# Kernel tuning notes

Hardware: AMD Instinct MI355X
Metric: run time of the kernel (lower is better)

The kernel has to match this reference:

```python
import jax, jax.numpy as jnp
import numpy as np

# dims: batch, nodes, d_node, d_edge, d_attn_hid, heads, d_node_hid, d_edge_hid, layers
B, N, DN, DE, DH, H, DNH, DEH, L = 2, 256, 128, 64, 128, 8, 512, 256, 2
DHH = DH // H  # per-head dim
SCALE = 1.0 / (DH ** 0.5)  # source scales by full d_hid, not per-head dim


def _ln(x, g, b):
    m = jnp.mean(x, -1, keepdims=True)
    v = jnp.mean((x - m) ** 2, -1, keepdims=True)
    return (x - m) * jax.lax.rsqrt(v + 1e-5) * g + b


def _gelu(x):
    return jax.nn.gelu(x, approximate=False)  # torch nn.GELU default = exact erf


def setup_inputs() -> dict:
    key = jax.random.key(0)
    ks = iter(jax.random.split(key, 40))
    def w(shape, scale=0.02):
        return jax.random.normal(next(ks), shape, jnp.float32) * scale
    return {
        "node_features": jax.random.normal(next(ks), (B, N, DN), jnp.float32),
        "edge_features": jax.random.normal(next(ks), (B, N, N, DE), jnp.float32),
        "Wqkv_n": w((L, DN, 3 * DH)),
        "Wqkv_e": w((L, DE, 4 * DH)),
        "Wo": w((L, DH, DN)), "bo": jnp.zeros((L, DN), jnp.float32),
        "Wl0": w((L, DN, DN)), "bl0": jnp.zeros((L, DN), jnp.float32),
        "ln0_g": jnp.ones((L, DN), jnp.float32), "ln0_b": jnp.zeros((L, DN), jnp.float32),
        "Wm1": w((L, DN, DNH)), "Wm2": w((L, DNH, DN)), "bm2": jnp.zeros((L, DN), jnp.float32),
        "ln1_g": jnp.ones((L, DN), jnp.float32), "ln1_b": jnp.zeros((L, DN), jnp.float32),
        "We0": w((L, 2 * DE, DEH)), "be0": jnp.zeros((L, DEH), jnp.float32),
        "Ws": w((L, DN, DEH)), "bs": jnp.zeros((L, DEH), jnp.float32),
        "Wt": w((L, DN, DEH)), "bt": jnp.zeros((L, DEH), jnp.float32),
        "We1": w((L, DEH, DE)), "be1": jnp.zeros((L, DE), jnp.float32),
        "eln0_g": jnp.ones((L, DE), jnp.float32), "eln0_b": jnp.zeros((L, DE), jnp.float32),
        "Wem1": w((L, DE, DEH)), "Wem2": w((L, DEH, DE)), "bem2": jnp.zeros((L, DE), jnp.float32),
        "eln1_g": jnp.ones((L, DE), jnp.float32), "eln1_b": jnp.zeros((L, DE), jnp.float32),
    }


def _forward(node_features, edge_features, Wqkv_n, Wqkv_e, Wo, bo, Wl0, bl0,
             ln0_g, ln0_b, Wm1, Wm2, bm2, ln1_g, ln1_b, We0, be0, Ws, bs, Wt, bt,
             We1, be1, eln0_g, eln0_b, Wem1, Wem2, bem2, eln1_g, eln1_b):
    x, e = node_features, edge_features
    for l in range(L):
        # --- RTAttention (modulate_v=True, eval mode) ---
        qkv_n = (x @ Wqkv_n[l]).reshape(B, N, H, 3 * DHH).transpose(0, 2, 1, 3)  # b h n 3d
        qn, kn, vn = jnp.split(qkv_n, 3, axis=-1)
        qkv_e = (e @ Wqkv_e[l]).reshape(B, N, N, H, 4 * DHH).transpose(0, 3, 1, 2, 4)  # b h i j 4d
        eq, ek, ev, em = jnp.split(qkv_e, 4, axis=-1)
        q = qn[:, :, :, None, :] + eq            # b h i j d
        k = kn[:, :, None, :, :] + ek            # b h i j d
        v = vn[:, :, None, :, :] * em + ev       # modulated values
        dots = SCALE * jnp.einsum('bhijd,bhijd->bhij', q, k)
        attn = jax.nn.softmax(dots, axis=-1)
        out = jnp.einsum('bhij,bhijd->bhid', attn, v)
        out = out.transpose(0, 2, 1, 3).reshape(B, N, DH)
        attn_out = out @ Wo[l] + bo[l]
        # --- node updates: ln(x + lin0(attn)); ln(x + mlp(x)) ---
        x = _ln(x + (attn_out @ Wl0[l] + bl0[l]), ln0_g[l], ln0_b[l])
        x = _ln(x + (_gelu(x @ Wm1[l]) @ Wm2[l] + bm2[l]), ln1_g[l], ln1_b[l])
        # --- edge updates (EdgeLayer) ---
        src = (x @ Ws[l] + bs[l])[:, :, None, :]   # broadcast over target j
        tgt = (x @ Wt[l] + bt[l])[:, None, :, :]   # broadcast over source i
        ecat = jnp.concatenate([e, e.transpose(0, 2, 1, 3)], axis=-1)  # [e_ij, e_ji]
        h = _gelu(ecat @ We0[l] + be0[l] + src + tgt)
        e = _ln(e + (h @ We1[l] + be1[l]), eln0_g[l], eln0_b[l])
        e = _ln(e + (_gelu(e @ Wem1[l]) @ Wem2[l] + bem2[l]), eln1_g[l], eln1_b[l])
    return x, e


def reference(node_features, edge_features, Wqkv_n, Wqkv_e, Wo, bo, Wl0, bl0,
              ln0_g, ln0_b, Wm1, Wm2, bm2, ln1_g, ln1_b, We0, be0, Ws, bs, Wt, bt,
              We1, be1, eln0_g, eln0_b, Wem1, Wem2, bem2, eln1_g, eln1_b):
    return _forward(node_features, edge_features, Wqkv_n, Wqkv_e, Wo, bo, Wl0, bl0,
                    ln0_g, ln0_b, Wm1, Wm2, bm2, ln1_g, ln1_b, We0, be0, Ws, bs, Wt, bt,
                    We1, be1, eln0_g, eln0_b, Wem1, Wem2, bem2, eln1_g, eln1_b)
```

## Files before the change

kernel.cpp:

```cpp
#include <hip/hip_runtime.h>
#include <hip/hip_bf16.h>
#include <stdint.h>

#define BB 2
#define NN 256
#define DN 128
#define DE 64
#define DH 128
#define NH 8
#define DHH 16
#define DNH 512
#define DEH 256
#define NL 2
#define SCALE_ATT 0.08838834764831845f

typedef __hip_bfloat16 bf16;
typedef __attribute__((ext_vector_type(8))) short short8;
typedef __attribute__((ext_vector_type(4))) float f32x4;

__device__ __forceinline__ float gelu_f(float x) {
  return 0.5f * x * (1.0f + erff(x * 0.70710678118654752f));
}
__device__ __forceinline__ float gelu_t(float x) {
  float m2u = x * fmaf(x * x, -0.07135481627f, -1.59576912161f);
  float e = __expf(m2u);
  return x * __builtin_amdgcn_rcpf(1.f + e);
}

__device__ __forceinline__ float wave_sum(float v) {
#pragma unroll
  for (int o = 32; o > 0; o >>= 1) v += __shfl_xor(v, o, 64);
  return v;
}

__device__ __forceinline__ short f2bf(float f) {
  union { float f; uint32_t u; } v{f};
  uint32_t r = (v.u + 0x7FFFu + ((v.u >> 16) & 1u)) >> 16;
  return (short)r;
}
__device__ __forceinline__ float bf2f(short s) {
  union { uint32_t u; float f; } v;
  v.u = ((uint32_t)(uint16_t)s) << 16;
  return v.f;
}

__device__ __forceinline__ int hswz(int m, int n) {
  return m * 256 + (n ^ ((m & 7) << 3));
}

__global__ void k_detect(const uint32_t* g8, const uint32_t* g13, int* flag) {
  if (threadIdx.x == 0 && blockIdx.x == 0) {
    uint32_t a = g8[0], b = g13[0];
    *flag = (a == 0x3F803F80u || b == 0x3F803F80u) ? 1 : 0;
  }
}

struct CastArgs {
  const void* src[30];
  float* dst[30];
  int n[30];
  const int* flag;
};

__global__ __launch_bounds__(256) void k_cast_all(CastArgs a) {
  int ti = blockIdx.y;
  float* d = a.dst[ti];
  int n = a.n[ti];
  int stride = gridDim.x * blockDim.x;
  if (*a.flag) {
    const bf16* s = (const bf16*)a.src[ti];
    for (int i = blockIdx.x * blockDim.x + threadIdx.x; i < n; i += stride)
      d[i] = __bfloat162float(s[i]);
  } else {
    const float* s = (const float*)a.src[ti];
    for (int i = blockIdx.x * blockDim.x + threadIdx.x; i < n; i += stride)
      d[i] = s[i];
  }
}

__global__ __launch_bounds__(256) void k_cast_e(const void* __restrict__ src,
                                                short* __restrict__ dst,
                                                const int* __restrict__ flag) {
  const int n8 = BB * NN * NN * DE / 8;
  int stride = gridDim.x * blockDim.x;
  if (*flag) {
    const uint4* s = (const uint4*)src;
    uint4* d = (uint4*)dst;
    for (int i = blockIdx.x * blockDim.x + threadIdx.x; i < n8; i += stride) d[i] = s[i];
  } else {
    const float4* s = (const float4*)src;
    for (int i = blockIdx.x * blockDim.x + threadIdx.x; i < n8; i += stride) {
      float4 a = s[2 * i], b = s[2 * i + 1];
      short* o = dst + 8 * i;
      o[0] = f2bf(a.x); o[1] = f2bf(a.y); o[2] = f2bf(a.z); o[3] = f2bf(a.w);
      o[4] = f2bf(b.x); o[5] = f2bf(b.y); o[6] = f2bf(b.z); o[7] = f2bf(b.w);
    }
  }
}

__global__ __launch_bounds__(256) void k_cast_out(const float* __restrict__ x,
                                                  const short* __restrict__ e,
                                                  void* __restrict__ out_v,
                                                  const int* __restrict__ flag) {
  const int nx = BB * NN * DN;
  const int total = nx + BB * NN * NN * DE;
  int stride = gridDim.x * blockDim.x;
  if (*flag) {
    short* out = (short*)out_v;
    for (int i = blockIdx.x * blockDim.x + threadIdx.x; i < total; i += stride)
      out[i] = (i < nx) ? f2bf(x[i]) : e[i - nx];
  } else {
    float* out = (float*)out_v;
    for (int i = blockIdx.x * blockDim.x + threadIdx.x; i < total; i += stride)
      out[i] = (i < nx) ? x[i] : bf2f(e[i - nx]);
  }
}

struct WtJob { const float* src; short* dst; int K; int N; };
struct WtArgs { WtJob job[10]; };
__global__ __launch_bounds__(256) void k_wtrans_all(WtArgs a) {
  WtJob j = a.job[blockIdx.y];
  int total = j.K * j.N;
  int stride = gridDim.x * 256;
  for (int idx = blockIdx.x * 256 + threadIdx.x; idx < total; idx += stride) {
    int k = idx / j.N, n = idx - k * j.N;
    j.dst[n * j.K + k] = f2bf(j.src[idx]);
  }
}

__global__ __launch_bounds__(128) void k_node_qkv(const float* __restrict__ x,
                                                  const float* __restrict__ W,
                                                  float* __restrict__ qkv) {
  int row = blockIdx.x;
  __shared__ float xs[DN];
  int t = threadIdx.x;
  xs[t] = x[row * DN + t];
  __syncthreads();
#pragma unroll
  for (int c0 = 0; c0 < 384; c0 += 128) {
    int c = c0 + t;
    float a = 0.f;
    for (int k = 0; k < DN; ++k) a = fmaf(xs[k], W[k * 384 + c], a);
    qkv[row * 384 + c] = a;
  }
}

__global__ __launch_bounds__(256) void k_attn_fused(
    const short* __restrict__ e, const short* __restrict__ WqeT,
    const float* __restrict__ qkv, float* __restrict__ o_buf) {
  int i = blockIdx.x, hs = blockIdx.y, b = blockIdx.z;
  __shared__ float sp[4 * NN];
  int t = threadIdx.x;
  int wv = t >> 6, lane = t & 63, g8 = lane >> 4, lo = lane & 15;
  int h = hs * 4 + wv;
  const short* erow = e + (size_t)(b * NN + i) * NN * DE;
  size_t qbase = (size_t)(b * NN) * 384;

  float qv = qkv[(size_t)(b * NN + i) * 384 + h * 48 + lo];

  {
    short8 bq[2][2];
#pragma unroll
    for (int p = 0; p < 2; ++p)
#pragma unroll
      for (int ks = 0; ks < 2; ++ks)
        bq[p][ks] = *(const short8*)(
            WqeT + (size_t)((h * 4 + p) * 16 + lo) * 64 + ks * 32 + g8 * 8);
#pragma unroll 2
    for (int mt = 0; mt < 16; ++mt) {
      const short* ea = erow + (mt * 16 + lo) * DE;
      short8 a0 = *(const short8*)(ea + g8 * 8);
      short8 a1 = *(const short8*)(ea + 32 + g8 * 8);
      float kn4[4];
#pragma unroll
      for (int r = 0; r < 4; ++r)
        kn4[r] = qkv[qbase + (size_t)(mt * 16 + g8 * 4 + r) * 384 + h * 48 + 16 + lo];
      f32x4 cq = {0.f, 0.f, 0.f, 0.f}, ck = {0.f, 0.f, 0.f, 0.f};
      cq = __builtin_amdgcn_mfma_f32_16x16x32_bf16(a0, bq[0][0], cq, 0, 0, 0);
      cq = __builtin_amdgcn_mfma_f32_16x16x32_bf16(a1, bq[0][1], cq, 0, 0, 0);
      ck = __builtin_amdgcn_mfma_f32_16x16x32_bf16(a0, bq[1][0], ck, 0, 0, 0);
      ck = __builtin_amdgcn_mfma_f32_16x16x32_bf16(a1, bq[1][1], ck, 0, 0, 0);
#pragma unroll
      for (int r = 0; r < 4; ++r) {
        int j = mt * 16 + g8 * 4 + r;
        float s = (qv + cq[r]) * (kn4[r] + ck[r]);
#pragma unroll
        for (int off = 1; off < 16; off <<= 1) s += __shfl_xor(s, off, 64);
        if (lo == 0) sp[wv * NN + j] = s * SCALE_ATT;
      }
    }
  }

  {
    float v[4];
#pragma unroll
    for (int q = 0; q < 4; ++q) v[q] = sp[wv * NN + lane + 64 * q];
    float m = fmaxf(fmaxf(v[0], v[1]), fmaxf(v[2], v[3]));
#pragma unroll
    for (int o = 32; o > 0; o >>= 1) m = fmaxf(m, __shfl_xor(m, o, 64));
    float l = 0.f;
#pragma unroll
    for (int q = 0; q < 4; ++q) { v[q] = __expf(v[q] - m); l += v[q]; }
    l = wave_sum(l);
    float inv = 1.f / l;
#pragma unroll
    for (int q = 0; q < 4; ++q) sp[wv * NN + lane + 64 * q] = v[q] * inv;
  }

  {
    short8 bv[2][2];
#pragma unroll
    for (int p = 0; p < 2; ++p)
#pragma unroll
      for (int ks = 0; ks < 2; ++ks)
        bv[p][ks] = *(const short8*)(
            WqeT + (size_t)((h * 4 + 2 + p) * 16 + lo) * 64 + ks * 32 + g8 * 8);
    float oacc = 0.f;
#pragma unroll 2
    for (int mt = 0; mt < 16; ++mt) {
      const short* ea = erow + (mt * 16 + lo) * DE;
      short8 a0 = *(const short8*)(ea + g8 * 8);
      short8 a1 = *(const short8*)(ea + 32 + g8 * 8);
      float vn4[4];
#pragma unroll
      for (int r = 0; r < 4; ++r)
        vn4[r] = qkv[qbase + (size_t)(mt * 16 + g8 * 4 + r) * 384 + h * 48 + 32 + lo];
      f32x4 cv = {0.f, 0.f, 0.f, 0.f}, cm = {0.f, 0.f, 0.f, 0.f};
      cv = __builtin_amdgcn_mfma_f32_16x16x32_bf16(a0, bv[0][0], cv, 0, 0, 0);
      cv = __builtin_amdgcn_mfma_f32_16x16x32_bf16(a1, bv[0][1], cv, 0, 0, 0);
      cm = __builtin_amdgcn_mfma_f32_16x16x32_bf16(a0, bv[1][0], cm, 0, 0, 0);
      cm = __builtin_amdgcn_mfma_f32_16x16x32_bf16(a1, bv[1][1], cm, 0, 0, 0);
#pragma unroll
      for (int r = 0; r < 4; ++r) {
        int j = mt * 16 + g8 * 4 + r;
        float vv = fmaf(vn4[r], cm[r], cv[r]);
        oacc = fmaf(sp[wv * NN + j], vv, oacc);
      }
    }
    oacc += __shfl_xor(oacc, 16, 64);
    oacc += __shfl_xor(oacc, 32, 64);
    if (g8 == 0) o_buf[(size_t)(b * NN + i) * DH + h * 16 + lo] = oacc;
  }
}

__global__ __launch_bounds__(128) void k_node_fused(
    const float* __restrict__ o_buf,
    const float* __restrict__ Wo, const float* __restrict__ bo,
    const float* __restrict__ Wl0, const float* __restrict__ bl0,
    const float* __restrict__ g0, const float* __restrict__ b0n,
    const float* __restrict__ Wm1, const float* __restrict__ Wm2,
    const float* __restrict__ bm2, const float* __restrict__ g1,
    const float* __restrict__ b1n, const float* __restrict__ Ws,
    const float* __restrict__ bs, const float* __restrict__ Wt,
    const float* __restrict__ bt, const float* __restrict__ WqnN,
    float* __restrict__ qkv, float* __restrict__ srcb,
    float* __restrict__ tgtb, float* __restrict__ x) {
  int i = blockIdx.x, b = blockIdx.y;
  int row = b * NN + i;
  __shared__ float orow[DH];
  __shared__ float t1[DH];
  __shared__ float xs[DN];
  __shared__ float hs[DNH];
  __shared__ float red[4];
  int t = threadIdx.x;
  orow[t] = o_buf[(size_t)row * DH + t];
  __syncthreads();
  {
    float a = bo[t];
    for (int k = 0; k < DH; ++k) a = fmaf(orow[k], Wo[k * DN + t], a);
    t1[t] = a;
  }
  __syncthreads();
  {
    float y = bl0[t] + x[row * DN + t];
    for (int k = 0; k < DN; ++k) y = fmaf(t1[k], Wl0[k * DN + t], y);
    float s1 = wave_sum(y), s2 = wave_sum(y * y);
    if ((t & 63) == 0) { red[t >> 6] = s1; red[2 + (t >> 6)] = s2; }
    __syncthreads();
    float mean = (red[0] + red[1]) * (1.f / 128.f);
    float var = (red[2] + red[3]) * (1.f / 128.f) - mean * mean;
    float rr = rsqrtf(var + 1e-5f);
    xs[t] = (y - mean) * rr * g0[t] + b0n[t];
  }
  __syncthreads();
#pragma unroll
  for (int p = 0; p < 4; ++p) {
    int c = t + 128 * p;
    float a = 0.f;
    for (int k = 0; k < DN; ++k) a = fmaf(xs[k], Wm1[k * DNH + c], a);
    hs[c] = gelu_f(a);
  }
  __syncthreads();
  {
    float y = bm2[t] + xs[t];
    for (int k = 0; k < DNH; ++k) y = fmaf(hs[k], Wm2[k * DN + t], y);
    float s1 = wave_sum(y), s2 = wave_sum(y * y);
    if ((t & 63) == 0) { red[t >> 6] = s1; red[2 + (t >> 6)] = s2; }
    __syncthreads();
    float mean = (red[0] + red[1]) * (1.f / 128.f);
    float var = (red[2] + red[3]) * (1.f / 128.f) - mean * mean;
    float rr = rsqrtf(var + 1e-5f);
    float x2 = (y - mean) * rr * g1[t] + b1n[t];
    x[row * DN + t] = x2;
    xs[t] = x2;
  }
  __syncthreads();
#pragma unroll
  for (int half = 0; half < 2; ++half) {
    int c = t + 128 * half;
    float a = bs[c], cc = bt[c];
    for (int k = 0; k < DN; ++k) {
      float xv = xs[k];
      a = fmaf(xv, Ws[k * DEH + c], a);
      cc = fmaf(xv, Wt[k * DEH + c], cc);
    }
    srcb[(size_t)row * DEH + c] = a;
    tgtb[(size_t)row * DEH + c] = cc;
  }
  if (WqnN) {
#pragma unroll
    for (int p = 0; p < 3; ++p) {
      int c = t + 128 * p;
      float a = 0.f;
      for (int k = 0; k < DN; ++k) a = fmaf(xs[k], WqnN[k * 384 + c], a);
      qkv[(size_t)row * 384 + c] = a;
    }
  }
}

__global__ __launch_bounds__(256) void k_edge_fused(
    const short* __restrict__ e_in, const short* __restrict__ W0T,
    const float* __restrict__ b0, const short* __restrict__ W1T,
    const float* __restrict__ b1, const float* __restrict__ srcb,
    const float* __restrict__ tgtb, const float* __restrict__ g,
    const float* __restrict__ bb, const short* __restrict__ Wm1T,
    const short* __restrict__ Wm2T, const float* __restrict__ bm2,
    const float* __restrict__ gm, const float* __restrict__ bbm,
    short* __restrict__ e_out) {
  int jt = blockIdx.x, i = blockIdx.y, b = blockIdx.z;
  int j0 = jt * 64;
  __shared__ short hidT[64 * 256];
  int t = threadIdx.x;
  int wv = t >> 6, lane = t & 63, g8 = lane >> 4, lo = lane & 15;
  int nq = wv * 64;
  int m0 = wv * 16;

  {
    float bias_n[4];
#pragma unroll
    for (int nt = 0; nt < 4; ++nt)
      bias_n[nt] = b0[nq + nt * 16 + lo] + srcb[(size_t)(b * NN + i) * DEH + nq + nt * 16 + lo];
    short8 bfr1[4][4];
#pragma unroll
    for (int nt = 0; nt < 4; ++nt)
#pragma unroll
      for (int ks = 0; ks < 4; ++ks)
        bfr1[nt][ks] =
            *(const short8*)(W0T + (size_t)(nq + nt * 16 + lo) * 128 + ks * 32 + g8 * 8);
#pragma unroll
    for (int mt = 0; mt < 4; ++mt) {
      int mrow = mt * 16 + lo;
      float tg[4][4];
#pragma unroll
      for (int nt = 0; nt < 4; ++nt)
#pragma unroll
        for (int r = 0; r < 4; ++r)
          tg[nt][r] = tgtb[((size_t)(b * NN) + j0 + mt * 16 + g8 * 4 + r) * DEH +
                           nq + nt * 16 + lo];
      short8 a[4];
      const short* eA = e_in + ((size_t)(b * NN + i) * NN + j0 + mrow) * DE;
#pragma unroll
      for (int ks = 0; ks < 2; ++ks) a[ks] = *(const short8*)(eA + ks * 32 + g8 * 8);
      const short* eT = e_in + ((size_t)(b * NN + j0 + mrow) * NN + i) * DE;
#pragma unroll
      for (int ks = 0; ks < 2; ++ks) a[2 + ks] = *(const short8*)(eT + ks * 32 + g8 * 8);
      f32x4 acc[4];
#pragma unroll
      for (int nt = 0; nt < 4; ++nt) {
        f32x4 c = {0.f, 0.f, 0.f, 0.f};
#pragma unroll
        for (int ks = 0; ks < 4; ++ks)
          c = __builtin_amdgcn_mfma_f32_16x16x32_bf16(a[ks], bfr1[nt][ks], c, 0, 0, 0);
        acc[nt] = c;
      }
#pragma unroll
      for (int nt = 0; nt < 4; ++nt) {
        int n = nq + nt * 16 + lo;
#pragma unroll
        for (int r = 0; r < 4; ++r) {
          int m = mt * 16 + g8 * 4 + r;
          hidT[hswz(m, n)] = f2bf(gelu_t(acc[nt][r] + bias_n[nt] + tg[nt][r]));
        }
      }
    }
  }
  __syncthreads();

  float emid[4][4];
  {
    float resv[4][4];
#pragma unroll
    for (int nt = 0; nt < 4; ++nt)
#pragma unroll
      for (int r = 0; r < 4; ++r)
        resv[nt][r] = bf2f(e_in[((size_t)(b * NN + i) * NN + j0 + m0 + g8 * 4 + r) * DE +
                                nt * 16 + lo]);
    short8 a2[8];
#pragma unroll
    for (int ks = 0; ks < 8; ++ks)
      a2[ks] = *(const short8*)(hidT + hswz(m0 + lo, ks * 32 + g8 * 8));
    f32x4 acc2[4];
#pragma unroll
    for (int nt = 0; nt < 4; ++nt) {
      f32x4 c = {0.f, 0.f, 0.f, 0.f};
      const short* bp = W1T + (size_t)(nt * 16 + lo) * 256;
#pragma unroll
      for (int ks = 0; ks < 8; ++ks)
        c = __builtin_amdgcn_mfma_f32_16x16x32_bf16(
            a2[ks], *(const short8*)(bp + ks * 32 + g8 * 8), c, 0, 0, 0);
      acc2[nt] = c;
    }
#pragma unroll
    for (int nt = 0; nt < 4; ++nt) {
      int n = nt * 16 + lo;
      float bb1 = b1[n];
#pragma unroll
      for (int r = 0; r < 4; ++r) emid[nt][r] = acc2[nt][r] + bb1 + resv[nt][r];
    }
#pragma unroll
    for (int r = 0; r < 4; ++r) {
      float s = emid[0][r] + emid[1][r] + emid[2][r] + emid[3][r];
      float q = emid[0][r] * emid[0][r] + emid[1][r] * emid[1][r] +
                emid[2][r] * emid[2][r] + emid[3][r] * emid[3][r];
#pragma unroll
      for (int off = 1; off < 16; off <<= 1) {
        s += __shfl_xor(s, off, 64);
        q += __shfl_xor(q, off, 64);
      }
      float mean = s * (1.f / 64.f);
      float var = q * (1.f / 64.f) - mean * mean;
      float rr = rsqrtf(var + 1e-5f);
      int m = m0 + g8 * 4 + r;
#pragma unroll
      for (int nt = 0; nt < 4; ++nt) {
        int n = nt * 16 + lo;
        float v = (emid[nt][r] - mean) * rr * g[n] + bb[n];
        emid[nt][r] = v;
        hidT[hswz(m, n)] = f2bf(v);
      }
    }
  }

  {
    short8 a3[2];
#pragma unroll
    for (int ks = 0; ks < 2; ++ks)
      a3[ks] = *(const short8*)(hidT + hswz(m0 + lo, ks * 32 + g8 * 8));
#pragma unroll 4
    for (int nt = 0; nt < 16; ++nt) {
      f32x4 c = {0.f, 0.f, 0.f, 0.f};
      const short* bp = Wm1T + (size_t)(nt * 16 + lo) * 64;
#pragma unroll
      for (int ks = 0; ks < 2; ++ks)
        c = __builtin_amdgcn_mfma_f32_16x16x32_bf16(
            a3[ks], *(const short8*)(bp + ks * 32 + g8 * 8), c, 0, 0, 0);
      int n = nt * 16 + lo;
#pragma unroll
      for (int r = 0; r < 4; ++r)
        hidT[hswz(m0 + g8 * 4 + r, n)] = f2bf(gelu_t(c[r]));
    }
  }

  {
    short8 a4[8];
#pragma unroll
    for (int ks = 0; ks < 8; ++ks)
      a4[ks] = *(const short8*)(hidT + hswz(m0 + lo, ks * 32 + g8 * 8));
    f32x4 acc4[4];
#pragma unroll
    for (int nt = 0; nt < 4; ++nt) {
      f32x4 c = {0.f, 0.f, 0.f, 0.f};
      const short* bp = Wm2T + (size_t)(nt * 16 + lo) * 256;
#pragma unroll
      for (int ks = 0; ks < 8; ++ks)
        c = __builtin_amdgcn_mfma_f32_16x16x32_bf16(
            a4[ks], *(const short8*)(bp + ks * 32 + g8 * 8), c, 0, 0, 0);
      acc4[nt] = c;
    }
    float vals[4][4];
#pragma unroll
    for (int nt = 0; nt < 4; ++nt) {
      int n = nt * 16 + lo;
      float bv = bm2[n];
#pragma unroll
      for (int r = 0; r < 4; ++r) vals[nt][r] = acc4[nt][r] + bv + emid[nt][r];
    }
#pragma unroll
    for (int r = 0; r < 4; ++r) {
      float s = vals[0][r] + vals[1][r] + vals[2][r] + vals[3][r];
      float q = vals[0][r] * vals[0][r] + vals[1][r] * vals[1][r] +
                vals[2][r] * vals[2][r] + vals[3][r] * vals[3][r];
#pragma unroll
      for (int off = 1; off < 16; off <<= 1) {
        s += __shfl_xor(s, off, 64);
        q += __shfl_xor(q, off, 64);
      }
      float mean = s * (1.f / 64.f);
      float var = q * (1.f / 64.f) - mean * mean;
      float rr = rsqrtf(var + 1e-5f);
      int m = m0 + g8 * 4 + r;
#pragma unroll
      for (int nt = 0; nt < 4; ++nt) {
        int n = nt * 16 + lo;
        e_out[((size_t)(b * NN + i) * NN + j0 + m) * DE + n] =
            f2bf((vals[nt][r] - mean) * rr * gm[n] + bbm[n]);
      }
    }
  }
}

extern "C" void kernel_launch(void* const* d_in, const int* in_sizes, int n_in,
                              void* d_out, int out_size, void* d_ws, size_t ws_size,
                              hipStream_t stream) {
  float* ws = (float*)d_ws;
  int* flag = (int*)ws;
  size_t off = 64;
  auto alloc = [&](size_t n) {
    float* p = ws + off;
    off += (n + 63) & ~(size_t)63;
    return p;
  };
  float* x_f = alloc((size_t)BB * NN * DN);
  short* e_a = (short*)alloc((size_t)BB * NN * NN * DE / 2);
  short* e_b = (short*)alloc((size_t)BB * NN * NN * DE / 2);
  float* qkv = alloc((size_t)BB * NN * 384);
  float* o_buf = alloc((size_t)BB * NN * DH);
  float* srcb = alloc((size_t)BB * NN * DEH);
  float* tgtb = alloc((size_t)BB * NN * DEH);
  short* WqeT = (short*)alloc(NL * 512 * 64 / 2);
  short* We0T = (short*)alloc(NL * 256 * 128 / 2);
  short* We1T = (short*)alloc(NL * 64 * 256 / 2);
  short* Wem1T = (short*)alloc(NL * 256 * 64 / 2);
  short* Wem2T = (short*)alloc(NL * 64 * 256 / 2);

  float* wf[30];
  wf[0] = x_f;
  wf[1] = x_f;
  CastArgs ca;
  int ntens = n_in < 30 ? n_in : 30;
  for (int idx = 0; idx < ntens; ++idx) {
    if (idx >= 2) wf[idx] = alloc((size_t)in_sizes[idx]);
    ca.src[idx] = d_in[idx];
    ca.dst[idx] = wf[idx];
    ca.n[idx] = (idx == 1) ? 0 : in_sizes[idx];
  }
  ca.flag = flag;

  k_detect<<<1, 64, 0, stream>>>((const uint32_t*)d_in[8], (const uint32_t*)d_in[13], flag);
  k_cast_all<<<dim3(64, ntens), dim3(256), 0, stream>>>(ca);
  k_cast_e<<<1024, 256, 0, stream>>>(d_in[1], e_a, flag);
  WtArgs wa;
  for (int l = 0; l < NL; ++l) {
    wa.job[l * 5 + 0] = {wf[3] + (size_t)l * DE * 512, WqeT + (size_t)l * 512 * 64, DE, 512};
    wa.job[l * 5 + 1] = {wf[15] + (size_t)l * 128 * 256, We0T + (size_t)l * 256 * 128, 128, 256};
    wa.job[l * 5 + 2] = {wf[21] + (size_t)l * 256 * 64, We1T + (size_t)l * 64 * 256, 256, 64};
    wa.job[l * 5 + 3] = {wf[25] + (size_t)l * 64 * 256, Wem1T + (size_t)l * 256 * 64, 64, 256};
    wa.job[l * 5 + 4] = {wf[26] + (size_t)l * 64 * 256, Wem2T + (size_t)l * 64 * 256, 256, 64};
  }
  k_wtrans_all<<<dim3(64, 10), 256, 0, stream>>>(wa);

  k_node_qkv<<<BB * NN, 128, 0, stream>>>(x_f, wf[2], qkv);

  for (int l = 0; l < NL; ++l) {
    const float* Wo = wf[4] + (size_t)l * DH * DN;
    const float* bo = wf[5] + (size_t)l * DN;
    const float* Wl0 = wf[6] + (size_t)l * DN * DN;
    const float* bl0 = wf[7] + (size_t)l * DN;
    const float* g0 = wf[8] + (size_t)l * DN;
    const float* b0n = wf[9] + (size_t)l * DN;
    const float* Wm1 = wf[10] + (size_t)l * DN * DNH;
    const float* Wm2 = wf[11] + (size_t)l * DNH * DN;
    const float* bm2 = wf[12] + (size_t)l * DN;
    const float* g1 = wf[13] + (size_t)l * DN;
    const float* b1n = wf[14] + (size_t)l * DN;
    const float* be0 = wf[16] + (size_t)l * DEH;
    const float* Wsw = wf[17] + (size_t)l * DN * DEH;
    const float* bsw = wf[18] + (size_t)l * DEH;
    const float* Wtw = wf[19] + (size_t)l * DN * DEH;
    const float* btw = wf[20] + (size_t)l * DEH;
    const float* be1 = wf[22] + (size_t)l * DE;
    const float* eg0 = wf[23] + (size_t)l * DE;
    const float* eb0 = wf[24] + (size_t)l * DE;
    const float* bem2 = wf[27] + (size_t)l * DE;
    const float* eg1 = wf[28] + (size_t)l * DE;
    const float* eb1 = wf[29] + (size_t)l * DE;
    const float* WqnNext = (l + 1 < NL) ? (wf[2] + (size_t)(l + 1) * DN * 3 * DH) : nullptr;

    const short* e_cur = (l == 0) ? e_a : e_b;
    short* e_nxt = (l == 0) ? e_b : e_a;

    k_attn_fused<<<dim3(NN, 2, BB), 256, 0, stream>>>(
        e_cur, WqeT + (size_t)l * 512 * 64, qkv, o_buf);
    k_node_fused<<<dim3(NN, BB), 128, 0, stream>>>(
        o_buf, Wo, bo, Wl0, bl0, g0, b0n, Wm1, Wm2, bm2, g1, b1n,
        Wsw, bsw, Wtw, btw, WqnNext, qkv, srcb, tgtb, x_f);
    k_edge_fused<<<dim3(NN / 64, NN, BB), 256, 0, stream>>>(
        e_cur, We0T + (size_t)l * 256 * 128, be0, We1T + (size_t)l * 64 * 256, be1,
        srcb, tgtb, eg0, eb0,
        Wem1T + (size_t)l * 256 * 64, Wem2T + (size_t)l * 64 * 256, bem2, eg1, eb1,
        e_nxt);
  }
  k_cast_out<<<1024, 256, 0, stream>>>(x_f, e_a, d_out, flag);
}
```

Measured before the change: 640.5 us.

## Transpose qkv and tgt buffers for vector loads; use DPP row reductions

```diff
diff --git a/kernel.cpp b/kernel.cpp
--- a/kernel.cpp
+++ b/kernel.cpp
@@ -12,6 +12,7 @@
 #define DNH 512
 #define DEH 256
 #define NL 2
+#define BN (BB * NN)
 #define SCALE_ATT 0.08838834764831845f
 
 typedef __hip_bfloat16 bf16;
@@ -27,9 +28,35 @@
   return x * __builtin_amdgcn_rcpf(1.f + e);
 }
 
+template <int ctrl>
+__device__ __forceinline__ float dppf(float v) {
+  return __int_as_float(
+      __builtin_amdgcn_update_dpp(0, __float_as_int(v), ctrl, 0xF, 0xF, true));
+}
+__device__ __forceinline__ float row_sum16(float v) {
+  v += dppf<0xB1>(v);
+  v += dppf<0x4E>(v);
+  v += dppf<0x124>(v);
+  v += dppf<0x128>(v);
+  return v;
+}
+__device__ __forceinline__ float row_max16(float v) {
+  v = fmaxf(v, dppf<0xB1>(v));
+  v = fmaxf(v, dppf<0x4E>(v));
+  v = fmaxf(v, dppf<0x124>(v));
+  v = fmaxf(v, dppf<0x128>(v));
+  return v;
+}
 __device__ __forceinline__ float wave_sum(float v) {
-#pragma unroll
-  for (int o = 32; o > 0; o >>= 1) v += __shfl_xor(v, o, 64);
+  v = row_sum16(v);
+  v += __shfl_xor(v, 16, 64);
+  v += __shfl_xor(v, 32, 64);
+  return v;
+}
+__device__ __forceinline__ float wave_max(float v) {
+  v = row_max16(v);
+  v = fmaxf(v, __shfl_xor(v, 16, 64));
+  v = fmaxf(v, __shfl_xor(v, 32, 64));
   return v;
 }
 
@@ -130,7 +157,7 @@
 
 __global__ __launch_bounds__(128) void k_node_qkv(const float* __restrict__ x,
                                                   const float* __restrict__ W,
-                                                  float* __restrict__ qkv) {
+                                                  float* __restrict__ qkvT) {
   int row = blockIdx.x;
   __shared__ float xs[DN];
   int t = threadIdx.x;
@@ -141,22 +168,21 @@
     int c = c0 + t;
     float a = 0.f;
     for (int k = 0; k < DN; ++k) a = fmaf(xs[k], W[k * 384 + c], a);
-    qkv[row * 384 + c] = a;
+    qkvT[(size_t)c * BN + row] = a;
   }
 }
 
 __global__ __launch_bounds__(256) void k_attn_fused(
     const short* __restrict__ e, const short* __restrict__ WqeT,
-    const float* __restrict__ qkv, float* __restrict__ o_buf) {
+    const float* __restrict__ qkvT, float* __restrict__ o_buf) {
   int i = blockIdx.x, hs = blockIdx.y, b = blockIdx.z;
   __shared__ float sp[4 * NN];
   int t = threadIdx.x;
   int wv = t >> 6, lane = t & 63, g8 = lane >> 4, lo = lane & 15;
   int h = hs * 4 + wv;
   const short* erow = e + (size_t)(b * NN + i) * NN * DE;
-  size_t qbase = (size_t)(b * NN) * 384;
-
-  float qv = qkv[(size_t)(b * NN + i) * 384 + h * 48 + lo];
+
+  float qv = qkvT[(size_t)(h * 48 + lo) * BN + b * NN + i];
 
   {
     short8 bq[2][2];
@@ -171,10 +197,8 @@
       const short* ea = erow + (mt * 16 + lo) * DE;
       short8 a0 = *(const short8*)(ea + g8 * 8);
       short8 a1 = *(const short8*)(ea + 32 + g8 * 8);
-      float kn4[4];
-#pragma unroll
-      for (int r = 0; r < 4; ++r)
-        kn4[r] = qkv[qbase + (size_t)(mt * 16 + g8 * 4 + r) * 384 + h * 48 + 16 + lo];
+      f32x4 kn4 = *(const f32x4*)(
+          qkvT + (size_t)(h * 48 + 16 + lo) * BN + b * NN + mt * 16 + g8 * 4);
       f32x4 cq = {0.f, 0.f, 0.f, 0.f}, ck = {0.f, 0.f, 0.f, 0.f};
       cq = __builtin_amdgcn_mfma_f32_16x16x32_bf16(a0, bq[0][0], cq, 0, 0, 0);
       cq = __builtin_amdgcn_mfma_f32_16x16x32_bf16(a1, bq[0][1], cq, 0, 0, 0);
@@ -184,8 +208,7 @@
       for (int r = 0; r < 4; ++r) {
         int j = mt * 16 + g8 * 4 + r;
         float s = (qv + cq[r]) * (kn4[r] + ck[r]);
-#pragma unroll
-        for (int off = 1; off < 16; off <<= 1) s += __shfl_xor(s, off, 64);
+        s = row_sum16(s);
         if (lo == 0) sp[wv * NN + j] = s * SCALE_ATT;
       }
     }
@@ -196,8 +219,7 @@
 #pragma unroll
     for (int q = 0; q < 4; ++q) v[q] = sp[wv * NN + lane + 64 * q];
     float m = fmaxf(fmaxf(v[0], v[1]), fmaxf(v[2], v[3]));
-#pragma unroll
-    for (int o = 32; o > 0; o >>= 1) m = fmaxf(m, __shfl_xor(m, o, 64));
+    m = wave_max(m);
     float l = 0.f;
 #pragma unroll
     for (int q = 0; q < 4; ++q) { v[q] = __expf(v[q] - m); l += v[q]; }
@@ -221,10 +243,8 @@
       const short* ea = erow + (mt * 16 + lo) * DE;
       short8 a0 = *(const short8*)(ea + g8 * 8);
       short8 a1 = *(const short8*)(ea + 32 + g8 * 8);
-      float vn4[4];
-#pragma unroll
-      for (int r = 0; r < 4; ++r)
-        vn4[r] = qkv[qbase + (size_t)(mt * 16 + g8 * 4 + r) * 384 + h * 48 + 32 + lo];
+      f32x4 vn4 = *(const f32x4*)(
+          qkvT + (size_t)(h * 48 + 32 + lo) * BN + b * NN + mt * 16 + g8 * 4);
       f32x4 cv = {0.f, 0.f, 0.f, 0.f}, cm = {0.f, 0.f, 0.f, 0.f};
       cv = __builtin_amdgcn_mfma_f32_16x16x32_bf16(a0, bv[0][0], cv, 0, 0, 0);
       cv = __builtin_amdgcn_mfma_f32_16x16x32_bf16(a1, bv[0][1], cv, 0, 0, 0);
@@ -253,8 +273,8 @@
     const float* __restrict__ b1n, const float* __restrict__ Ws,
     const float* __restrict__ bs, const float* __restrict__ Wt,
     const float* __restrict__ bt, const float* __restrict__ WqnN,
-    float* __restrict__ qkv, float* __restrict__ srcb,
-    float* __restrict__ tgtb, float* __restrict__ x) {
+    float* __restrict__ qkvT, float* __restrict__ srcb,
+    float* __restrict__ tgtbT, float* __restrict__ x) {
   int i = blockIdx.x, b = blockIdx.y;
   int row = b * NN + i;
   __shared__ float orow[DH];
@@ -315,7 +335,7 @@
       cc = fmaf(xv, Wt[k * DEH + c], cc);
     }
     srcb[(size_t)row * DEH + c] = a;
-    tgtb[(size_t)row * DEH + c] = cc;
+    tgtbT[(size_t)c * BN + row] = cc;
   }
   if (WqnN) {
 #pragma unroll
@@ -323,7 +343,7 @@
       int c = t + 128 * p;
       float a = 0.f;
       for (int k = 0; k < DN; ++k) a = fmaf(xs[k], WqnN[k * 384 + c], a);
-      qkv[(size_t)row * 384 + c] = a;
+      qkvT[(size_t)c * BN + row] = a;
     }
   }
 }
@@ -332,7 +352,7 @@
     const short* __restrict__ e_in, const short* __restrict__ W0T,
     const float* __restrict__ b0, const short* __restrict__ W1T,
     const float* __restrict__ b1, const float* __restrict__ srcb,
-    const float* __restrict__ tgtb, const float* __restrict__ g,
+    const float* __restrict__ tgtbT, const float* __restrict__ g,
     const float* __restrict__ bb, const short* __restrict__ Wm1T,
     const short* __restrict__ Wm2T, const float* __restrict__ bm2,
     const float* __restrict__ gm, const float* __restrict__ bbm,
@@ -360,13 +380,11 @@
 #pragma unroll
     for (int mt = 0; mt < 4; ++mt) {
       int mrow = mt * 16 + lo;
-      float tg[4][4];
+      f32x4 tgv[4];
 #pragma unroll
       for (int nt = 0; nt < 4; ++nt)
-#pragma unroll
-        for (int r = 0; r < 4; ++r)
-          tg[nt][r] = tgtb[((size_t)(b * NN) + j0 + mt * 16 + g8 * 4 + r) * DEH +
-                           nq + nt * 16 + lo];
+        tgv[nt] = *(const f32x4*)(
+            tgtbT + (size_t)(nq + nt * 16 + lo) * BN + b * NN + j0 + mt * 16 + g8 * 4);
       short8 a[4];
       const short* eA = e_in + ((size_t)(b * NN + i) * NN + j0 + mrow) * DE;
 #pragma unroll
@@ -389,7 +407,7 @@
 #pragma unroll
         for (int r = 0; r < 4; ++r) {
           int m = mt * 16 + g8 * 4 + r;
-          hidT[hswz(m, n)] = f2bf(gelu_t(acc[nt][r] + bias_n[nt] + tg[nt][r]));
+          hidT[hswz(m, n)] = f2bf(gelu_t(acc[nt][r] + bias_n[nt] + tgv[nt][r]));
         }
       }
     }
@@ -432,11 +450,8 @@
       float s = emid[0][r] + emid[1][r] + emid[2][r] + emid[3][r];
       float q = emid[0][r] * emid[0][r] + emid[1][r] * emid[1][r] +
                 emid[2][r] * emid[2][r] + emid[3][r] * emid[3][r];
-#pragma unroll
-      for (int off = 1; off < 16; off <<= 1) {
-        s += __shfl_xor(s, off, 64);
-        q += __shfl_xor(q, off, 64);
-      }
+      s = row_sum16(s);
+      q = row_sum16(q);
       float mean = s * (1.f / 64.f);
       float var = q * (1.f / 64.f) - mean * mean;
       float rr = rsqrtf(var + 1e-5f);
@@ -500,11 +515,8 @@
       float s = vals[0][r] + vals[1][r] + vals[2][r] + vals[3][r];
       float q = vals[0][r] * vals[0][r] + vals[1][r] * vals[1][r] +
                 vals[2][r] * vals[2][r] + vals[3][r] * vals[3][r];
-#pragma unroll
-      for (int off = 1; off < 16; off <<= 1) {
-        s += __shfl_xor(s, off, 64);
-        q += __shfl_xor(q, off, 64);
-      }
+      s = row_sum16(s);
+      q = row_sum16(q);
       float mean = s * (1.f / 64.f);
       float var = q * (1.f / 64.f) - mean * mean;
       float rr = rsqrtf(var + 1e-5f);
@@ -533,10 +545,10 @@
   float* x_f = alloc((size_t)BB * NN * DN);
   short* e_a = (short*)alloc((size_t)BB * NN * NN * DE / 2);
   short* e_b = (short*)alloc((size_t)BB * NN * NN * DE / 2);
-  float* qkv = alloc((size_t)BB * NN * 384);
+  float* qkvT = alloc((size_t)384 * BN);
   float* o_buf = alloc((size_t)BB * NN * DH);
   float* srcb = alloc((size_t)BB * NN * DEH);
-  float* tgtb = alloc((size_t)BB * NN * DEH);
+  float* tgtbT = alloc((size_t)DEH * BN);
   short* WqeT = (short*)alloc(NL * 512 * 64 / 2);
   short* We0T = (short*)alloc(NL * 256 * 128 / 2);
   short* We1T = (short*)alloc(NL * 64 * 256 / 2);
@@ -569,7 +581,7 @@
   }
   k_wtrans_all<<<dim3(64, 10), 256, 0, stream>>>(wa);
 
-  k_node_qkv<<<BB * NN, 128, 0, stream>>>(x_f, wf[2], qkv);
+  k_node_qkv<<<BB * NN, 128, 0, stream>>>(x_f, wf[2], qkvT);
 
   for (int l = 0; l < NL; ++l) {
     const float* Wo = wf[4] + (size_t)l * DH * DN;
@@ -600,13 +612,13 @@
     short* e_nxt = (l == 0) ? e_b : e_a;
 
     k_attn_fused<<<dim3(NN, 2, BB), 256, 0, stream>>>(
-        e_cur, WqeT + (size_t)l * 512 * 64, qkv, o_buf);
+        e_cur, WqeT + (size_t)l * 512 * 64, qkvT, o_buf);
     k_node_fused<<<dim3(NN, BB), 128, 0, stream>>>(
         o_buf, Wo, bo, Wl0, bl0, g0, b0n, Wm1, Wm2, bm2, g1, b1n,
-        Wsw, bsw, Wtw, btw, WqnNext, qkv, srcb, tgtb, x_f);
+        Wsw, bsw, Wtw, btw, WqnNext, qkvT, srcb, tgtbT, x_f);
     k_edge_fused<<<dim3(NN / 64, NN, BB), 256, 0, stream>>>(
         e_cur, We0T + (size_t)l * 256 * 128, be0, We1T + (size_t)l * 64 * 256, be1,
-        srcb, tgtb, eg0, eb0,
+        srcb, tgtbT, eg0, eb0,
         Wem1T + (size_t)l * 256 * 64, Wem2T + (size_t)l * 64 * 256, bem2, eg1, eb1,
         e_nxt);
   }
```

Measured after the change: 664.1 us. 1.04x slower.
